# Kernel tuning notes

Measured on AMD Instinct MI355X. Metric: run time of the kernel, lower is better.

## Reference

```python
import jax, jax.numpy as jnp
import numpy as np

BETA = 5.5  # exp-cosine kernel sharpness (module default)

def _l2norm(x, axis=-1):
    return x / jnp.linalg.norm(x, axis=axis, keepdims=True)

def setup_inputs() -> dict:
    key = jax.random.key(0)
    ks = jax.random.split(key, 7)
    C, Mt, D = 1000, 33, 1024  # classes, memory slots (32 learned + 1 fixed), feat dim
    img_feat = jax.random.normal(ks[0], (1, D), jnp.float32)
    memory = jax.random.normal(ks[1], (C, Mt, D), jnp.float32)
    # simulate unfilled memory slots (exercises the zero-row masking branch)
    memory = memory.at[:, 24:32, :].set(0.0)
    global_bias = jax.random.normal(ks[2], (C, D), jnp.float32) * 0.02
    global_bias_key = jax.random.normal(ks[3], (C, D), jnp.float32) * 0.02
    global_bias_value = jax.random.normal(ks[4], (C, D), jnp.float32) * 0.02
    global_ffn_bias = jax.random.normal(ks[5], (C, D), jnp.float32) * 0.02
    logit_scale = jnp.ones((1,), jnp.float32) * jnp.log(100.0).astype(jnp.float32)
    return {
        "img_feat": img_feat,
        "memory": memory,
        "global_bias": global_bias,
        "global_bias_key": global_bias_key,
        "global_bias_value": global_bias_value,
        "global_ffn_bias": global_ffn_bias,
        "logit_scale": logit_scale,
    }

def reference(img_feat, memory, global_bias, global_bias_key, global_bias_value,
              global_ffn_bias, logit_scale):
    # position == 'all', center_type_clip == 'attn'
    # query: image feature shifted by mean class bias, L2-normalized
    q = _l2norm(img_feat + jnp.mean(global_bias, axis=0, keepdims=True))  # [1, D]
    # keys / values: per-class bias add + L2 norm, with empty slots zeroed
    empty = (jnp.sum(memory, axis=-1) == 0)[..., None]                    # [C, Mt, 1]
    K = jnp.where(empty, 0.0, _l2norm(memory + global_bias_key[:, None, :]))
    V = jnp.where(empty, 0.0, _l2norm(memory + global_bias_value[:, None, :]))
    # exp-cosine similarity kernel: exp(-beta * (1 - cos))
    sim = jnp.einsum('d,cmd->cm', q[0], K)                                # [C, Mt]
    sim = jnp.exp(-BETA * (1.0 - sim))
    # weighted sum over memory slots, renormalize, output bias, renormalize
    a = _l2norm(jnp.einsum('cm,cmd->cd', sim, V))                          # [C, D]
    a = _l2norm(a + global_ffn_bias)
    logits = jnp.exp(logit_scale[0]) * (a @ img_feat[0])                   # [C]
    return jax.nn.softmax(logits)[None, :]                                 # [1, C]
```

## Files before the change

kernel.cpp:

```cpp
#include <hip/hip_runtime.h>
#include <math.h>

#define NCLS 1000
#define MT 33
#define D 1024
#define BETA 5.5f

__device__ __forceinline__ float wave_sum(float v) {
#pragma unroll
  for (int off = 32; off; off >>= 1) v += __shfl_xor(v, off, 64);
  return v;
}

__device__ __forceinline__ float dot4(float4 a, float4 b) {
  return a.x * b.x + a.y * b.y + a.z * b.z + a.w * b.w;
}

__device__ __forceinline__ float block_sum16(float v, volatile float* scr) {
  v = wave_sum(v);
  const int wv = threadIdx.x >> 6, lane = threadIdx.x & 63;
  if (lane == 0) scr[wv] = v;
  __syncthreads();
  if (wv == 0) {
    float x = (lane < 16) ? scr[lane] : 0.0f;
#pragma unroll
    for (int off = 8; off; off >>= 1) x += __shfl_xor(x, off, 64);
    if (lane == 0) scr[16] = x;
  }
  __syncthreads();
  return scr[16];
}

__device__ __forceinline__ float2 block_sum2(float a, float b, volatile float* scr) {
  a = wave_sum(a);
  b = wave_sum(b);
  const int wv = threadIdx.x >> 6, lane = threadIdx.x & 63;
  if (lane == 0) {
    scr[wv] = a;
    scr[16 + wv] = b;
  }
  __syncthreads();
  if (wv == 0) {
    float x = (lane < 16) ? scr[lane] : 0.0f;
    float y = (lane < 16) ? scr[16 + lane] : 0.0f;
#pragma unroll
    for (int off = 8; off; off >>= 1) {
      x += __shfl_xor(x, off, 64);
      y += __shfl_xor(y, off, 64);
    }
    if (lane == 0) {
      scr[32] = x;
      scr[33] = y;
    }
  }
  __syncthreads();
  return make_float2(scr[32], scr[33]);
}

__global__ __launch_bounds__(1024) void zero_kernel(float* __restrict__ s) {
  s[threadIdx.x] = 0.0f;
}

__global__ __launch_bounds__(1024) void colsum_kernel(const float* __restrict__ gb,
                                                      float* __restrict__ s) {
  const int t = threadIdx.x;
  float p = 0.0f;
  for (int c = blockIdx.x; c < NCLS; c += gridDim.x) p += gb[(size_t)c * D + t];
  atomicAdd(&s[t], p);
}

__global__ __launch_bounds__(1024) void main_kernel(
    const float* __restrict__ memp, const float* __restrict__ gbk,
    const float* __restrict__ gbv, const float* __restrict__ gffn,
    const float* __restrict__ img, const float* __restrict__ s,
    const float* __restrict__ ls, float* __restrict__ logits) {
  __shared__ float red[8 * D];
  __shared__ float scr[40];
  const int c = blockIdx.x;
  const int t = threadIdx.x;
  const int wv = t >> 6, lane = t & 63;
  const int dbase = lane * 4;

  const float* gbk_c = gbk + (size_t)c * D;
  const float* gbv_c = gbv + (size_t)c * D;

  float4 qv[4], kv[4], vvr[4];
  float qss = 0.0f;
#pragma unroll
  for (int k = 0; k < 4; ++k) {
    const int d = k * 256 + dbase;
    const float4 iv = *(const float4*)(img + d);
    const float4 sv = *(const float4*)(s + d);
    float4 v;
    v.x = iv.x + sv.x * (1.0f / (float)NCLS);
    v.y = iv.y + sv.y * (1.0f / (float)NCLS);
    v.z = iv.z + sv.z * (1.0f / (float)NCLS);
    v.w = iv.w + sv.w * (1.0f / (float)NCLS);
    qv[k] = v;
    qss += dot4(v, v);
    kv[k] = *(const float4*)(gbk_c + d);
    vvr[k] = *(const float4*)(gbv_c + d);
  }
  qss = wave_sum(qss);
  const float qinv = 1.0f / sqrtf(qss);
#pragma unroll
  for (int k = 0; k < 4; ++k) {
    qv[k].x *= qinv; qv[k].y *= qinv; qv[k].z *= qinv; qv[k].w *= qinv;
  }

  float kk = 0.0f, vv2 = 0.0f, qk = 0.0f;
#pragma unroll
  for (int k = 0; k < 4; ++k) {
    kk += dot4(kv[k], kv[k]);
    vv2 += dot4(vvr[k], vvr[k]);
    qk += dot4(qv[k], kv[k]);
  }
  kk = wave_sum(kk);
  vv2 = wave_sum(vv2);
  qk = wave_sum(qk);

  float4 acc[4];
#pragma unroll
  for (int k = 0; k < 4; ++k) acc[k] = make_float4(0.f, 0.f, 0.f, 0.f);
  float Wsum = 0.0f;

  const float* memc = memp + (size_t)c * MT * D;
  for (int m = wv; m < MT; m += 16) {
    float4 mv[4];
#pragma unroll
    for (int k = 0; k < 4; ++k)
      mv[k] = *(const float4*)(memc + (size_t)m * D + k * 256 + dbase);
    float pqm = 0.f, pkm = 0.f, pvm = 0.f, pmm = 0.f;
#pragma unroll
    for (int k = 0; k < 4; ++k) {
      pqm += dot4(qv[k], mv[k]);
      pkm += dot4(kv[k], mv[k]);
      pvm += dot4(vvr[k], mv[k]);
      pmm += dot4(mv[k], mv[k]);
    }
    pqm = wave_sum(pqm);
    pkm = wave_sum(pkm);
    pvm = wave_sum(pvm);
    pmm = wave_sum(pmm);

    const float nk = sqrtf(pmm + 2.0f * pkm + kk);
    const float cosv = (pqm + qk) / nk;
    const float sim = expf(-BETA * (1.0f - cosv));
    const float nv = sqrtf(pmm + 2.0f * pvm + vv2);
    const float wgt = (pmm == 0.0f) ? 0.0f : sim / nv;
    Wsum += wgt;
#pragma unroll
    for (int k = 0; k < 4; ++k) {
      acc[k].x += wgt * mv[k].x;
      acc[k].y += wgt * mv[k].y;
      acc[k].z += wgt * mv[k].z;
      acc[k].w += wgt * mv[k].w;
    }
  }
#pragma unroll
  for (int k = 0; k < 4; ++k) {
    acc[k].x += Wsum * vvr[k].x;
    acc[k].y += Wsum * vvr[k].y;
    acc[k].z += Wsum * vvr[k].z;
    acc[k].w += Wsum * vvr[k].w;
  }

  if (wv >= 8) {
    float* dst = red + (wv - 8) * D + dbase;
#pragma unroll
    for (int k = 0; k < 4; ++k) *(float4*)(dst + k * 256) = acc[k];
  }
  __syncthreads();
  if (wv < 8) {
    float* ptr = red + wv * D + dbase;
#pragma unroll
    for (int k = 0; k < 4; ++k) {
      const float4 t4 = *(const float4*)(ptr + k * 256);
      acc[k].x += t4.x;
      acc[k].y += t4.y;
      acc[k].z += t4.z;
      acc[k].w += t4.w;
    }
#pragma unroll
    for (int k = 0; k < 4; ++k) *(float4*)(ptr + k * 256) = acc[k];
  }
  __syncthreads();
  float araw = 0.0f;
#pragma unroll
  for (int w = 0; w < 8; ++w) araw += red[w * D + t];

  const float n1sq = block_sum16(araw * araw, scr);
  const float a1 = araw / sqrtf(n1sq) + gffn[(size_t)c * D + t];
  const float2 r2 = block_sum2(a1 * a1, a1 * img[t], scr);
  if (t == 0) logits[c] = expf(ls[0]) * r2.y / sqrtf(r2.x);
}

__global__ __launch_bounds__(1024) void softmax_kernel(const float* __restrict__ logits,
                                                       float* __restrict__ out) {
  __shared__ float scr[40];
  const int t = threadIdx.x;
  const int wv = t >> 6, lane = t & 63;
  const float l = (t < NCLS) ? logits[t] : -INFINITY;
  float m = l;
#pragma unroll
  for (int off = 32; off; off >>= 1) m = fmaxf(m, __shfl_xor(m, off, 64));
  if (lane == 0) scr[wv] = m;
  __syncthreads();
  if (wv == 0) {
    float x = (lane < 16) ? scr[lane] : -INFINITY;
#pragma unroll
    for (int off = 8; off; off >>= 1) x = fmaxf(x, __shfl_xor(x, off, 64));
    if (lane == 0) scr[16] = x;
  }
  __syncthreads();
  m = scr[16];
  const float e = (t < NCLS) ? expf(l - m) : 0.0f;
  const float sden = block_sum16(e, scr);
  if (t < NCLS) out[t] = e / sden;
}

extern "C" void kernel_launch(void* const* d_in, const int* in_sizes, int n_in,
                              void* d_out, int out_size, void* d_ws, size_t ws_size,
                              hipStream_t stream) {
  const float* img = (const float*)d_in[0];
  const float* memp = (const float*)d_in[1];
  const float* gb = (const float*)d_in[2];
  const float* gbk = (const float*)d_in[3];
  const float* gbv = (const float*)d_in[4];
  const float* gffn = (const float*)d_in[5];
  const float* ls = (const float*)d_in[6];
  float* out = (float*)d_out;

  float* s = (float*)d_ws;
  float* logits = s + D;

  zero_kernel<<<1, D, 0, stream>>>(s);
  colsum_kernel<<<64, D, 0, stream>>>(gb, s);
  main_kernel<<<NCLS, D, 0, stream>>>(memp, gbk, gbv, gffn, img, s, ls, logits);
  softmax_kernel<<<1, D, 0, stream>>>(logits, out);
}
```

Measured before the change: 237.0 us.

## Shrink main kernel to 4-wave blocks and replace block reductions with wave reductions

The main kernel now runs each class with 256 threads (4 waves) instead of 1024, so each wave handles about 8-9 memory slots instead of 2-3. With a single partial-sum pass through shared memory, every wave ends up holding the full aggregated vector, and the later normalizations and dot products need only wave shuffles rather than multi-barrier block reductions. The goal is less idle thread time (the old 16-wave layout left many waves with only 2 slots), fewer barriers, and more resident blocks per CU. In exchange, the per-wave slot loop is longer and serial, so latency hiding per block now depends more on having several blocks resident.

```diff
diff --git a/kernel.cpp b/kernel.cpp
--- a/kernel.cpp
+++ b/kernel.cpp
@@ -29,32 +29,6 @@
   }
   __syncthreads();
   return scr[16];
-}
-
-__device__ __forceinline__ float2 block_sum2(float a, float b, volatile float* scr) {
-  a = wave_sum(a);
-  b = wave_sum(b);
-  const int wv = threadIdx.x >> 6, lane = threadIdx.x & 63;
-  if (lane == 0) {
-    scr[wv] = a;
-    scr[16 + wv] = b;
-  }
-  __syncthreads();
-  if (wv == 0) {
-    float x = (lane < 16) ? scr[lane] : 0.0f;
-    float y = (lane < 16) ? scr[16 + lane] : 0.0f;
-#pragma unroll
-    for (int off = 8; off; off >>= 1) {
-      x += __shfl_xor(x, off, 64);
-      y += __shfl_xor(y, off, 64);
-    }
-    if (lane == 0) {
-      scr[32] = x;
-      scr[33] = y;
-    }
-  }
-  __syncthreads();
-  return make_float2(scr[32], scr[33]);
 }
 
 __global__ __launch_bounds__(1024) void zero_kernel(float* __restrict__ s) {
@@ -69,13 +43,12 @@
   atomicAdd(&s[t], p);
 }
 
-__global__ __launch_bounds__(1024) void main_kernel(
+__global__ __launch_bounds__(256, 4) void main_kernel(
     const float* __restrict__ memp, const float* __restrict__ gbk,
     const float* __restrict__ gbv, const float* __restrict__ gffn,
     const float* __restrict__ img, const float* __restrict__ s,
     const float* __restrict__ ls, float* __restrict__ logits) {
-  __shared__ float red[8 * D];
-  __shared__ float scr[40];
+  __shared__ float red[4][D];
   const int c = blockIdx.x;
   const int t = threadIdx.x;
   const int wv = t >> 6, lane = t & 63;
@@ -125,7 +98,7 @@
   float Wsum = 0.0f;
 
   const float* memc = memp + (size_t)c * MT * D;
-  for (int m = wv; m < MT; m += 16) {
+  for (int m = wv; m < MT; m += 4) {
     float4 mv[4];
 #pragma unroll
     for (int k = 0; k < 4; ++k)
@@ -165,34 +138,45 @@
     acc[k].w += Wsum * vvr[k].w;
   }
 
-  if (wv >= 8) {
-    float* dst = red + (wv - 8) * D + dbase;
-#pragma unroll
-    for (int k = 0; k < 4; ++k) *(float4*)(dst + k * 256) = acc[k];
-  }
-  __syncthreads();
-  if (wv < 8) {
-    float* ptr = red + wv * D + dbase;
-#pragma unroll
-    for (int k = 0; k < 4; ++k) {
-      const float4 t4 = *(const float4*)(ptr + k * 256);
-      acc[k].x += t4.x;
-      acc[k].y += t4.y;
-      acc[k].z += t4.z;
-      acc[k].w += t4.w;
-    }
-#pragma unroll
-    for (int k = 0; k < 4; ++k) *(float4*)(ptr + k * 256) = acc[k];
-  }
-  __syncthreads();
-  float araw = 0.0f;
-#pragma unroll
-  for (int w = 0; w < 8; ++w) araw += red[w * D + t];
-
-  const float n1sq = block_sum16(araw * araw, scr);
-  const float a1 = araw / sqrtf(n1sq) + gffn[(size_t)c * D + t];
-  const float2 r2 = block_sum2(a1 * a1, a1 * img[t], scr);
-  if (t == 0) logits[c] = expf(ls[0]) * r2.y / sqrtf(r2.x);
+#pragma unroll
+  for (int k = 0; k < 4; ++k) *(float4*)(&red[wv][k * 256 + dbase]) = acc[k];
+  __syncthreads();
+#pragma unroll
+  for (int k = 0; k < 4; ++k) {
+    const float4 a0 = *(const float4*)(&red[0][k * 256 + dbase]);
+    const float4 a1 = *(const float4*)(&red[1][k * 256 + dbase]);
+    const float4 a2 = *(const float4*)(&red[2][k * 256 + dbase]);
+    const float4 a3 = *(const float4*)(&red[3][k * 256 + dbase]);
+    acc[k].x = a0.x + a1.x + a2.x + a3.x;
+    acc[k].y = a0.y + a1.y + a2.y + a3.y;
+    acc[k].z = a0.z + a1.z + a2.z + a3.z;
+    acc[k].w = a0.w + a1.w + a2.w + a3.w;
+  }
+
+  float n1 = 0.0f;
+#pragma unroll
+  for (int k = 0; k < 4; ++k) n1 += dot4(acc[k], acc[k]);
+  n1 = wave_sum(n1);
+  const float inv1 = 1.0f / sqrtf(n1);
+
+  const float* gffn_c = gffn + (size_t)c * D;
+  float n2 = 0.0f, d3 = 0.0f;
+#pragma unroll
+  for (int k = 0; k < 4; ++k) {
+    const int d = k * 256 + dbase;
+    const float4 gf = *(const float4*)(gffn_c + d);
+    const float4 iv = *(const float4*)(img + d);
+    float4 a1v;
+    a1v.x = acc[k].x * inv1 + gf.x;
+    a1v.y = acc[k].y * inv1 + gf.y;
+    a1v.z = acc[k].z * inv1 + gf.z;
+    a1v.w = acc[k].w * inv1 + gf.w;
+    n2 += dot4(a1v, a1v);
+    d3 += dot4(a1v, iv);
+  }
+  n2 = wave_sum(n2);
+  d3 = wave_sum(d3);
+  if (t == 0) logits[c] = expf(ls[0]) * d3 / sqrtf(n2);
 }
 
 __global__ __launch_bounds__(1024) void softmax_kernel(const float* __restrict__ logits,
@@ -236,6 +220,6 @@
 
   zero_kernel<<<1, D, 0, stream>>>(s);
   colsum_kernel<<<64, D, 0, stream>>>(gb, s);
-  main_kernel<<<NCLS, D, 0, stream>>>(memp, gbk, gbv, gffn, img, s, ls, logits);
+  main_kernel<<<NCLS, 256, 0, stream>>>(memp, gbk, gbv, gffn, img, s, ls, logits);
   softmax_kernel<<<1, D, 0, stream>>>(logits, out);
 }
```

Measured after the change: 229.9 us. 1.03x faster.
